# Optimization experiments

Measured on AMD Instinct MI355X. Metric: run time of the kernel, lower is better.

The kernel has to match this reference:

```python
import jax, jax.numpy as jnp
import numpy as np

N_NODES = 100000
N_EDGES = 1600000


def setup_inputs() -> dict:
    key = jax.random.key(0)
    ks = jax.random.split(key, 6)
    x = jax.random.normal(ks[0], (N_NODES, 128), dtype=jnp.float32)
    src = jax.random.randint(ks[1], (N_EDGES,), 0, N_NODES, dtype=jnp.int32)
    dst = jax.random.randint(ks[2], (N_EDGES,), 0, N_NODES, dtype=jnp.int32)
    # Glorot-ish scaled weights
    W1 = jax.random.normal(ks[3], (128, 64), dtype=jnp.float32) / np.sqrt(128.0)
    b1 = jnp.zeros((64,), dtype=jnp.float32)
    W2 = jax.random.normal(ks[4], (64, 64), dtype=jnp.float32) / np.sqrt(64.0)
    b2 = jnp.zeros((64,), dtype=jnp.float32)
    return {"x": x, "src": src, "dst": dst, "W1": W1, "b1": b1, "W2": W2, "b2": b2}


def _gcn_forward(x, src_f, dst_f, norm_src, norm_dst, W1, b1, W2, b2):
    n = x.shape[0]

    def conv(h, W, b):
        # weight-first (in_feats >= out_feats in DGL GraphConv): h W is cheap, aggregate small dim
        h = h @ W                                  # [N, d_out]
        h = h * norm_src[:, None]                  # D_out^{-1/2} on source side
        msg = h[src_f]                             # gather per edge [E+N, d_out]
        agg = jax.ops.segment_sum(msg, dst_f, num_segments=n)  # scatter-add to dst
        return agg * norm_dst[:, None] + b         # D_in^{-1/2} + bias

    h = jax.nn.relu(conv(x, W1, b1))
    return conv(h, W2, b2)


def reference(x, src, dst, W1, b1, W2, b2):
    n = x.shape[0]
    loop = jnp.arange(n, dtype=src.dtype)
    src_f = jnp.concatenate([src, loop])  # dgl.add_self_loop
    dst_f = jnp.concatenate([dst, loop])
    ones = jnp.ones(src_f.shape[0], dtype=x.dtype)
    out_deg = jax.ops.segment_sum(ones, src_f, num_segments=n)
    in_deg = jax.ops.segment_sum(ones, dst_f, num_segments=n)
    norm_src = jax.lax.rsqrt(out_deg)  # deg >= 1 due to self loops
    norm_dst = jax.lax.rsqrt(in_deg)
    return _gcn_forward(x, src_f, dst_f, norm_src, norm_dst, W1, b1, W2, b2)
```

## Files before the change

### kernel.cpp

```cpp
#include <hip/hip_runtime.h>
#include <hip/hip_fp16.h>

#define D 64
#define SLICE 25000
#define NBUCK 512
#define EPB 4096

typedef __attribute__((ext_vector_type(8))) short short8;
typedef __attribute__((ext_vector_type(4))) float floatx4;

__global__ __launch_bounds__(1024) void k_hist(const int* __restrict__ src,
                                               const int* __restrict__ dst,
                                               int* __restrict__ cnt_out,
                                               int* __restrict__ cnt_in,
                                               int E, int N) {
    __shared__ int h[SLICE];
    const int* idx = blockIdx.z ? dst : src;
    int* cnt       = blockIdx.z ? cnt_in : cnt_out;
    int lo = blockIdx.y * SLICE;
    int hi = min(lo + SLICE, N);
    int len = hi - lo;
    for (int i = threadIdx.x; i < len; i += 1024) h[i] = 0;
    __syncthreads();

    const int E4 = E >> 2;
    const int4* idx4 = (const int4*)idx;
    int stride = gridDim.x * 1024;
    for (int i = blockIdx.x * 1024 + threadIdx.x; i < E4; i += stride) {
        int4 v = idx4[i];
        if (v.x >= lo && v.x < hi) atomicAdd(&h[v.x - lo], 1);
        if (v.y >= lo && v.y < hi) atomicAdd(&h[v.y - lo], 1);
        if (v.z >= lo && v.z < hi) atomicAdd(&h[v.z - lo], 1);
        if (v.w >= lo && v.w < hi) atomicAdd(&h[v.w - lo], 1);
    }
    if (blockIdx.x == 0) {
        int e = E4 * 4 + threadIdx.x;
        if (e < E) {
            int v = idx[e];
            if (v >= lo && v < hi) atomicAdd(&h[v - lo], 1);
        }
    }
    __syncthreads();
    for (int i = threadIdx.x; i < len; i += 1024) {
        int c = h[i];
        if (c) atomicAdd(&cnt[lo + i], c);
    }
}

__global__ __launch_bounds__(256) void k_norm(const int* __restrict__ cnt,
                                              float* __restrict__ nrm, int n) {
    int i = blockIdx.x * 256 + threadIdx.x;
    if (i < n) nrm[i] = rsqrtf((float)cnt[i] + 1.0f);
}

__global__ __launch_bounds__(256) void k_scan1(const int* __restrict__ in,
                                               int* __restrict__ out,
                                               int* __restrict__ partials, int n) {
    __shared__ int s[256];
    int tid = threadIdx.x;
    int base = blockIdx.x * 1024 + tid * 4;
    int v[4];
#pragma unroll
    for (int j = 0; j < 4; ++j) v[j] = (base + j < n) ? in[base + j] : 0;
    int l1 = v[0] + v[1];
    int l2 = l1 + v[2];
    int total = l2 + v[3];
    s[tid] = total;
    __syncthreads();
    for (int off = 1; off < 256; off <<= 1) {
        int add = (tid >= off) ? s[tid - off] : 0;
        __syncthreads();
        s[tid] += add;
        __syncthreads();
    }
    int excl = s[tid] - total;
    if (base + 0 < n) out[base + 0] = excl;
    if (base + 1 < n) out[base + 1] = excl + v[0];
    if (base + 2 < n) out[base + 2] = excl + l1;
    if (base + 3 < n) out[base + 3] = excl + l2;
    if (tid == 255) partials[blockIdx.x] = s[255];
}

__global__ void k_scan2(int* __restrict__ partials, int B,
                        int* __restrict__ row_ptr, int N, int E) {
    if (threadIdx.x == 0) {
        int run = 0;
        for (int i = 0; i < B; ++i) {
            int tmp = partials[i];
            partials[i] = run;
            run += tmp;
        }
    }
    if (threadIdx.x == 1) row_ptr[N] = E;
}

__global__ __launch_bounds__(256) void k_scan3(int* __restrict__ out,
                                               const int* __restrict__ partials, int n) {
    int off = partials[blockIdx.x];
    int base = blockIdx.x * 1024 + threadIdx.x * 4;
#pragma unroll
    for (int j = 0; j < 4; ++j)
        if (base + j < n) out[base + j] += off;
}

__global__ __launch_bounds__(256) void k_bin(const int* __restrict__ src,
                                             const int* __restrict__ dst,
                                             const int* __restrict__ row_ptr,
                                             int* __restrict__ bucket_cursor,
                                             unsigned long long* __restrict__ binned,
                                             int E) {
    __shared__ int cnt[NBUCK];
    __shared__ int bloc[NBUCK];
    __shared__ int lcur[NBUCK];
    __shared__ int gbase[NBUCK];
    __shared__ int ss[256];
    __shared__ unsigned long long stage[EPB];

    int tid = threadIdx.x;
    int start = blockIdx.x * EPB;
    int nloc = min(EPB, E - start);

    for (int i = tid; i < NBUCK; i += 256) cnt[i] = 0;
    __syncthreads();

#pragma unroll
    for (int r = 0; r < EPB / 256; ++r) {
        int idx = start + r * 256 + tid;
        if (idx < E) atomicAdd(&cnt[dst[idx] >> 8], 1);
    }
    __syncthreads();

    int a = cnt[2 * tid], b = cnt[2 * tid + 1];
    ss[tid] = a + b;
    __syncthreads();
    for (int off = 1; off < 256; off <<= 1) {
        int add = (tid >= off) ? ss[tid - off] : 0;
        __syncthreads();
        ss[tid] += add;
        __syncthreads();
    }
    int excl = ss[tid] - (a + b);
    bloc[2 * tid] = excl;           lcur[2 * tid] = excl;
    bloc[2 * tid + 1] = excl + a;   lcur[2 * tid + 1] = excl + a;
    __syncthreads();

    for (int bk = tid; bk < NBUCK; bk += 256) {
        int c = cnt[bk];
        gbase[bk] = c ? (atomicAdd(&bucket_cursor[bk], c) + row_ptr[bk << 8]) : 0;
    }
    __syncthreads();

#pragma unroll
    for (int r = 0; r < EPB / 256; ++r) {
        int idx = start + r * 256 + tid;
        if (idx < E) {
            int d = dst[idx];
            int p = atomicAdd(&lcur[d >> 8], 1);
            stage[p] = ((unsigned long long)(unsigned)d << 32) | (unsigned)src[idx];
        }
    }
    __syncthreads();

#pragma unroll
    for (int r = 0; r < EPB / 256; ++r) {
        int i = r * 256 + tid;
        if (i < nloc) {
            unsigned long long e = stage[i];
            int bk = (int)(e >> 40);
            binned[gbase[bk] + (i - bloc[bk])] = e;
        }
    }
}

__global__ __launch_bounds__(256) void k_bsort(const unsigned long long* __restrict__ binned,
                                               const int* __restrict__ row_ptr,
                                               int* __restrict__ csr, int N) {
    __shared__ int cur[256];
    int b = blockIdx.x;
    int n0 = b << 8;
    int tid = threadIdx.x;
    if (n0 + tid < N) cur[tid] = row_ptr[n0 + tid];
    __syncthreads();
    int base = row_ptr[n0];
    int c = row_ptr[min(n0 + 256, N)] - base;
    for (int k = tid; k < c; k += 256) {
        unsigned long long e = binned[base + k];
        int d = (int)(e >> 32);
        int s = (int)(e & 0xffffffffu);
        int p = atomicAdd(&cur[d - n0], 1);
        csr[p] = s;
    }
}

template <int K>
__global__ __launch_bounds__(256) void k_gemm_mfma(const float* __restrict__ hsrc,
                                                   const float* __restrict__ W,
                                                   const float* __restrict__ norm_src,
                                                   __half* __restrict__ t, int N) {
    constexpr int NKI = K / 32;
    __shared__ short Whi[NKI * 2048];
    __shared__ short Wlo[NKI * 2048];
    int tid = threadIdx.x;

    for (int f = tid; f < K * 64; f += 256) {
        int n  = f & 15;
        int j  = (f >> 4) & 7;
        int q  = (f >> 7) & 3;
        int ct = (f >> 9) & 3;
        int ki = f >> 11;
        int k = ki * 32 + q * 8 + j;
        int c = ct * 16 + n;
        float w = W[k * 64 + c];
        unsigned u = __float_as_uint(w);
        float l = w - __uint_as_float(u & 0xffff0000u);
        int idx = (((ki * 4 + ct) * 16 + n) * 4 + q) * 8 + j;
        Whi[idx] = (short)(u >> 16);
        Wlo[idx] = (short)(__float_as_uint(l) >> 16);
    }
    __syncthreads();

    int wave = tid >> 6, lane = tid & 63;
    int q = lane >> 4, n = lane & 15;
    int r0 = blockIdx.x * 64 + wave * 16;
    int rowc = min(r0 + n, N - 1);

    floatx4 acc[4] = {{0.f,0.f,0.f,0.f},{0.f,0.f,0.f,0.f},
                      {0.f,0.f,0.f,0.f},{0.f,0.f,0.f,0.f}};

    for (int ki = 0; ki < NKI; ++ki) {
        const float* ap = hsrc + (long long)rowc * K + ki * 32 + q * 8;
        float4 a0 = *(const float4*)ap;
        float4 a1 = *(const float4*)(ap + 4);
        float av[8] = {a0.x, a0.y, a0.z, a0.w, a1.x, a1.y, a1.z, a1.w};
        short8 ahi, alo;
#pragma unroll
        for (int j = 0; j < 8; ++j) {
            unsigned u = __float_as_uint(av[j]);
            float l = av[j] - __uint_as_float(u & 0xffff0000u);
            ahi[j] = (short)(u >> 16);
            alo[j] = (short)(__float_as_uint(l) >> 16);
        }
#pragma unroll
        for (int ct = 0; ct < 4; ++ct) {
            int bidx = (((ki * 4 + ct) * 16 + n) * 4 + q) * 8;
            short8 bhi = *(const short8*)&Whi[bidx];
            short8 blo = *(const short8*)&Wlo[bidx];
            acc[ct] = __builtin_amdgcn_mfma_f32_16x16x32_bf16(ahi, bhi, acc[ct], 0, 0, 0);
            acc[ct] = __builtin_amdgcn_mfma_f32_16x16x32_bf16(ahi, blo, acc[ct], 0, 0, 0);
            acc[ct] = __builtin_amdgcn_mfma_f32_16x16x32_bf16(alo, bhi, acc[ct], 0, 0, 0);
        }
    }

#pragma unroll
    for (int reg = 0; reg < 4; ++reg) {
        int orow = r0 + q * 4 + reg;
        if (orow < N) {
            float nrm = norm_src[orow];
#pragma unroll
            for (int ct = 0; ct < 4; ++ct)
                t[(long long)orow * 64 + ct * 16 + n] = __float2half(acc[ct][reg] * nrm);
        }
    }
}

__global__ __launch_bounds__(256) void k_agg(const int* __restrict__ row_ptr,
                                             const int* __restrict__ cnt,
                                             const int* __restrict__ csr,
                                             const __half* __restrict__ t,
                                             const float* __restrict__ norm_dst,
                                             const float* __restrict__ bias,
                                             float* __restrict__ out, int N, int do_relu) {
    int tid = threadIdx.x;
    int half_id = tid >> 5;
    int lane = tid & 31;
    int i = blockIdx.x * 8 + half_id;
    if (i >= N) return;
    const __half2* t2 = (const __half2*)t;
    int start = row_ptr[i], c = cnt[i];

    float2 sf = __half22float2(t2[i * 32 + lane]);
    float ax = sf.x, ay = sf.y;

    int j = 0;
    int pre = min(c, (4 - (start & 3)) & 3);
    for (; j < pre; ++j) {
        float2 f = __half22float2(t2[csr[start + j] * 32 + lane]);
        ax += f.x; ay += f.y;
    }
    for (; j + 4 <= c; j += 4) {
        int4 s4 = *(const int4*)&csr[start + j];
        float2 f0 = __half22float2(t2[s4.x * 32 + lane]);
        float2 f1 = __half22float2(t2[s4.y * 32 + lane]);
        float2 f2 = __half22float2(t2[s4.z * 32 + lane]);
        float2 f3 = __half22float2(t2[s4.w * 32 + lane]);
        ax += (f0.x + f1.x) + (f2.x + f3.x);
        ay += (f0.y + f1.y) + (f2.y + f3.y);
    }
    for (; j < c; ++j) {
        float2 f = __half22float2(t2[csr[start + j] * 32 + lane]);
        ax += f.x; ay += f.y;
    }

    float nrm = norm_dst[i];
    float2 bb = ((const float2*)bias)[lane];
    float vx = fmaf(ax, nrm, bb.x);
    float vy = fmaf(ay, nrm, bb.y);
    if (do_relu) { vx = fmaxf(vx, 0.f); vy = fmaxf(vy, 0.f); }
    float2 o; o.x = vx; o.y = vy;
    ((float2*)out)[i * 32 + lane] = o;
}

extern "C" void kernel_launch(void* const* d_in, const int* in_sizes, int n_in,
                              void* d_out, int out_size, void* d_ws, size_t ws_size,
                              hipStream_t stream) {
    const float* x   = (const float*)d_in[0];
    const int*   src = (const int*)d_in[1];
    const int*   dst = (const int*)d_in[2];
    const float* W1  = (const float*)d_in[3];
    const float* b1  = (const float*)d_in[4];
    const float* W2  = (const float*)d_in[5];
    const float* b2  = (const float*)d_in[6];
    float* out = (float*)d_out;

    const int N = in_sizes[0] / 128;
    const int E = in_sizes[1];

    int*   cnt_out  = (int*)d_ws;
    int*   cnt_in   = cnt_out + N;
    int*   row_ptr  = cnt_in + N;
    int*   partials = row_ptr + N + 1;
    float* norm_src = (float*)(partials + 1024);
    float* norm_dst = norm_src + N;
    long long toff = (5LL * N + 1025 + 63) & ~63LL;
    float* tbase    = (float*)d_ws + toff;
    float* h        = tbase + (long long)N * D;
    int*   csr      = (int*)(h + (long long)N * D);
    int*   bucket_cursor = csr + E;
    __half* t_h = (__half*)tbase;
    unsigned long long* binned = (unsigned long long*)tbase;

    const int B = (N + 1023) / 1024;
    const int NS = (N + SLICE - 1) / SLICE;
    const int NB = (N + 255) / 256;
    const int NBK = (E + EPB - 1) / EPB;

    hipMemsetAsync(cnt_out, 0, (size_t)2 * N * sizeof(int), stream);
    hipMemsetAsync(bucket_cursor, 0, (size_t)NBUCK * sizeof(int), stream);

    k_hist<<<dim3(8, NS, 2), 1024, 0, stream>>>(src, dst, cnt_out, cnt_in, E, N);
    k_norm<<<(2 * N + 255) / 256, 256, 0, stream>>>(cnt_out, norm_src, 2 * N);

    k_scan1<<<B, 256, 0, stream>>>(cnt_in, row_ptr, partials, N);
    k_scan2<<<1, 64, 0, stream>>>(partials, B, row_ptr, N, E);
    k_scan3<<<B, 256, 0, stream>>>(row_ptr, partials, N);

    k_bin<<<NBK, 256, 0, stream>>>(src, dst, row_ptr, bucket_cursor, binned, E);
    k_bsort<<<NB, 256, 0, stream>>>(binned, row_ptr, csr, N);

    k_gemm_mfma<128><<<(N + 63) / 64, 256, 0, stream>>>(x, W1, norm_src, t_h, N);
    k_agg<<<(N + 7) / 8, 256, 0, stream>>>(row_ptr, cnt_in, csr, t_h, norm_dst, b1, h, N, 1);

    k_gemm_mfma<64><<<(N + 63) / 64, 256, 0, stream>>>(h, W2, norm_src, t_h, N);
    k_agg<<<(N + 7) / 8, 256, 0, stream>>>(row_ptr, cnt_in, csr, t_h, norm_dst, b2, out, N, 0);
}
```

Baseline: 314.0 us.

## Fuse layer-1 aggregation with layer-2 GEMM into one kernel

Adds a kernel that aggregates 64 nodes' neighbor features into shared memory, applies norm, bias and ReLU, then multiplies by W2 with split-bf16 MFMA and writes the normalized fp16 layer-2 features. This removes the fp32 hidden-activation write and re-read plus one kernel launch. In exchange each block does both gather and GEMM, with a barrier between them and more shared memory (about 33 KB), which may lower occupancy during the latency-bound gather phase.

```diff
diff --git a/kernel.cpp b/kernel.cpp
--- a/kernel.cpp
+++ b/kernel.cpp
@@ -263,6 +263,113 @@
     }
 }
 
+__global__ __launch_bounds__(256) void k_aggmm(const int* __restrict__ row_ptr,
+                                               const int* __restrict__ cnt,
+                                               const int* __restrict__ csr,
+                                               const __half* __restrict__ t,
+                                               const float* __restrict__ norm_dst,
+                                               const float* __restrict__ norm_src,
+                                               const float* __restrict__ bias,
+                                               const float* __restrict__ W,
+                                               __half* __restrict__ t2, int N) {
+    __shared__ float hs[64][68];
+    __shared__ short Whi[4096];
+    __shared__ short Wlo[4096];
+    int tid = threadIdx.x;
+
+    for (int f = tid; f < 64 * 64; f += 256) {
+        int n  = f & 15;
+        int j  = (f >> 4) & 7;
+        int q  = (f >> 7) & 3;
+        int ct = (f >> 9) & 3;
+        int ki = f >> 11;
+        int k = ki * 32 + q * 8 + j;
+        int c = ct * 16 + n;
+        float w = W[k * 64 + c];
+        unsigned u = __float_as_uint(w);
+        float l = w - __uint_as_float(u & 0xffff0000u);
+        int idx = (((ki * 4 + ct) * 16 + n) * 4 + q) * 8 + j;
+        Whi[idx] = (short)(u >> 16);
+        Wlo[idx] = (short)(__float_as_uint(l) >> 16);
+    }
+
+    int hw = tid >> 5, lane = tid & 31;
+    const __half2* t2r = (const __half2*)t;
+    float2 bb = ((const float2*)bias)[lane];
+    for (int r = 0; r < 8; ++r) {
+        int il = r * 8 + hw;
+        int i = blockIdx.x * 64 + il;
+        if (i < N) {
+            int start = row_ptr[i], c = cnt[i];
+            float2 sf = __half22float2(t2r[i * 32 + lane]);
+            float ax = sf.x, ay = sf.y;
+            int j = 0;
+            int pre = min(c, (4 - (start & 3)) & 3);
+            for (; j < pre; ++j) {
+                float2 f = __half22float2(t2r[csr[start + j] * 32 + lane]);
+                ax += f.x; ay += f.y;
+            }
+            for (; j + 4 <= c; j += 4) {
+                int4 s4 = *(const int4*)&csr[start + j];
+                float2 f0 = __half22float2(t2r[s4.x * 32 + lane]);
+                float2 f1 = __half22float2(t2r[s4.y * 32 + lane]);
+                float2 f2 = __half22float2(t2r[s4.z * 32 + lane]);
+                float2 f3 = __half22float2(t2r[s4.w * 32 + lane]);
+                ax += (f0.x + f1.x) + (f2.x + f3.x);
+                ay += (f0.y + f1.y) + (f2.y + f3.y);
+            }
+            for (; j < c; ++j) {
+                float2 f = __half22float2(t2r[csr[start + j] * 32 + lane]);
+                ax += f.x; ay += f.y;
+            }
+            float nrm = norm_dst[i];
+            hs[il][lane * 2]     = fmaxf(fmaf(ax, nrm, bb.x), 0.f);
+            hs[il][lane * 2 + 1] = fmaxf(fmaf(ay, nrm, bb.y), 0.f);
+        }
+    }
+    __syncthreads();
+
+    int wave = tid >> 6, lane64 = tid & 63;
+    int q = lane64 >> 4, n = lane64 & 15;
+    int m = wave * 16 + n;
+    floatx4 acc[4] = {{0.f,0.f,0.f,0.f},{0.f,0.f,0.f,0.f},
+                      {0.f,0.f,0.f,0.f},{0.f,0.f,0.f,0.f}};
+#pragma unroll
+    for (int ki = 0; ki < 2; ++ki) {
+        const float* ap = &hs[m][ki * 32 + q * 8];
+        float4 a0 = *(const float4*)ap;
+        float4 a1 = *(const float4*)(ap + 4);
+        float av[8] = {a0.x, a0.y, a0.z, a0.w, a1.x, a1.y, a1.z, a1.w};
+        short8 ahi, alo;
+#pragma unroll
+        for (int j = 0; j < 8; ++j) {
+            unsigned u = __float_as_uint(av[j]);
+            float l = av[j] - __uint_as_float(u & 0xffff0000u);
+            ahi[j] = (short)(u >> 16);
+            alo[j] = (short)(__float_as_uint(l) >> 16);
+        }
+#pragma unroll
+        for (int ct = 0; ct < 4; ++ct) {
+            int bidx = (((ki * 4 + ct) * 16 + n) * 4 + q) * 8;
+            short8 bhi = *(const short8*)&Whi[bidx];
+            short8 blo = *(const short8*)&Wlo[bidx];
+            acc[ct] = __builtin_amdgcn_mfma_f32_16x16x32_bf16(ahi, bhi, acc[ct], 0, 0, 0);
+            acc[ct] = __builtin_amdgcn_mfma_f32_16x16x32_bf16(ahi, blo, acc[ct], 0, 0, 0);
+            acc[ct] = __builtin_amdgcn_mfma_f32_16x16x32_bf16(alo, bhi, acc[ct], 0, 0, 0);
+        }
+    }
+#pragma unroll
+    for (int reg = 0; reg < 4; ++reg) {
+        int orow = blockIdx.x * 64 + wave * 16 + q * 4 + reg;
+        if (orow < N) {
+            float nrm = norm_src[orow];
+#pragma unroll
+            for (int ct = 0; ct < 4; ++ct)
+                t2[(long long)orow * 64 + ct * 16 + n] = __float2half(acc[ct][reg] * nrm);
+        }
+    }
+}
+
 __global__ __launch_bounds__(256) void k_agg(const int* __restrict__ row_ptr,
                                              const int* __restrict__ cnt,
                                              const int* __restrict__ csr,
@@ -333,10 +440,11 @@
     float* norm_dst = norm_src + N;
     long long toff = (5LL * N + 1025 + 63) & ~63LL;
     float* tbase    = (float*)d_ws + toff;
-    float* h        = tbase + (long long)N * D;
-    int*   csr      = (int*)(h + (long long)N * D);
+    float* hreg     = tbase + (long long)N * D;
+    int*   csr      = (int*)(hreg + (long long)N * D);
     int*   bucket_cursor = csr + E;
-    __half* t_h = (__half*)tbase;
+    __half* t_h  = (__half*)tbase;
+    __half* t2_h = (__half*)hreg;
     unsigned long long* binned = (unsigned long long*)tbase;
 
     const int B = (N + 1023) / 1024;
@@ -358,8 +466,7 @@
     k_bsort<<<NB, 256, 0, stream>>>(binned, row_ptr, csr, N);
 
     k_gemm_mfma<128><<<(N + 63) / 64, 256, 0, stream>>>(x, W1, norm_src, t_h, N);
-    k_agg<<<(N + 7) / 8, 256, 0, stream>>>(row_ptr, cnt_in, csr, t_h, norm_dst, b1, h, N, 1);
-
-    k_gemm_mfma<64><<<(N + 63) / 64, 256, 0, stream>>>(h, W2, norm_src, t_h, N);
-    k_agg<<<(N + 7) / 8, 256, 0, stream>>>(row_ptr, cnt_in, csr, t_h, norm_dst, b2, out, N, 0);
-}
+    k_aggmm<<<(N + 63) / 64, 256, 0, stream>>>(row_ptr, cnt_in, csr, t_h,
+                                               norm_dst, norm_src, b1, W2, t2_h, N);
+    k_agg<<<(N + 7) / 8, 256, 0, stream>>>(row_ptr, cnt_in, csr, t2_h, norm_dst, b2, out, N, 0);
+}
```

Result: slower. 353.8 us (+12.7%).
